# Optimization experiments

Measured on AMD Instinct MI355X. Metric: run time of the kernel, lower is better.

Reference implementation:

```python
import jax, jax.numpy as jnp
import numpy as np

HEAD_SIZE = 64


def setup_inputs() -> dict:
    key = jax.random.key(0)
    ks = jax.random.split(key, 4)
    B, S, H, D = 8, 4096, 768, HEAD_SIZE
    scale = 1.0 / np.sqrt(H)
    return {
        "x": jax.random.normal(ks[0], (B, S, H), dtype=jnp.float32),
        "Wq": jax.random.normal(ks[1], (H, D), dtype=jnp.float32) * scale,
        "bq": jnp.zeros((D,), dtype=jnp.float32),
        "Wk": jax.random.normal(ks[2], (H, D), dtype=jnp.float32) * scale,
        "bk": jnp.zeros((D,), dtype=jnp.float32),
        "Wv": jax.random.normal(ks[3], (H, D), dtype=jnp.float32) * scale,
        "bv": jnp.zeros((D,), dtype=jnp.float32),
    }


def reference(x, Wq, bq, Wk, bk, Wv, bv):
    # x: [B, S, H]
    B, S, H = x.shape
    D = Wq.shape[1]
    q = x @ Wq + bq  # [B, S, D]
    k = x @ Wk + bk
    v = x @ Wv + bv
    # naive full score matrix [B, S, S]
    scores = jnp.einsum("bsd,btd->bst", q, k)
    causal = jnp.tril(jnp.ones((S, S), dtype=bool))  # lower-triangular mask
    scores = jnp.where(causal[None, :, :], scores, -jnp.inf)
    attn = jax.nn.softmax(scores / jnp.sqrt(jnp.float32(D)), axis=-1)
    # dropout is identity in eval/deterministic reference
    out = jnp.einsum("bst,btd->bsd", attn, v)  # [B, S, D]
    return out
```

## Files before the change

kernel.cpp:

```cpp
#include <hip/hip_runtime.h>

typedef unsigned short u16;
typedef __bf16 bf16_t;
typedef bf16_t bf16x8 __attribute__((ext_vector_type(8)));
typedef float f32x4 __attribute__((ext_vector_type(4)));
typedef u16 u16x8 __attribute__((ext_vector_type(8)));
typedef u16 u16x4 __attribute__((ext_vector_type(4)));
typedef unsigned u32x4 __attribute__((ext_vector_type(4)));

#define B_ 8
#define S_ 4096
#define H_ 768
#define M_ (B_ * S_)

__device__ __forceinline__ u16 f2b(float f) {
  unsigned u = __float_as_uint(f);
  u += 0x7fffu + ((u >> 16) & 1u);
  return (u16)(u >> 16);
}

__device__ __forceinline__ void gl_lds16(const void* g, void* l) {
  __builtin_amdgcn_global_load_lds(
      (const __attribute__((address_space(1))) void*)g,
      (__attribute__((address_space(3))) void*)l, 16, 0, 0);
}

__global__ __launch_bounds__(256) void wconv_k(const float* __restrict__ Wq,
                                               const float* __restrict__ Wk,
                                               const float* __restrict__ Wv,
                                               u16* __restrict__ WbT) {
  __shared__ float wt[64 * 68];
  const int tid = threadIdx.x;
  int mat = blockIdx.x / 12;
  int k0 = (blockIdx.x % 12) * 64;
  const float* W = (mat == 0) ? Wq : ((mat == 1) ? Wk : Wv);
  int r = tid >> 2, c0 = (tid & 3) * 16;
  const float* src = W + (size_t)(k0 + r) * 64 + c0;
#pragma unroll
  for (int j = 0; j < 16; j += 4)
    *(float4*)&wt[r * 68 + c0 + j] = *(const float4*)(src + j);
  __syncthreads();
  int d = tid >> 2;
  u16* dst = WbT + (size_t)(mat * 64 + d) * 768 + k0 + c0;
  u16x8 o0, o1;
#pragma unroll
  for (int j = 0; j < 8; ++j) o0[j] = f2b(wt[(c0 + j) * 68 + d]);
#pragma unroll
  for (int j = 0; j < 8; ++j) o1[j] = f2b(wt[(c0 + 8 + j) * 68 + d]);
  *(u16x8*)dst = o0;
  *(u16x8*)(dst + 8) = o1;
}

__global__ __launch_bounds__(512) void qkv_k(const float* __restrict__ x,
                                             const u16* __restrict__ WbT,
                                             const float* __restrict__ bq,
                                             const float* __restrict__ bk,
                                             const float* __restrict__ bv,
                                             u16* __restrict__ qb,
                                             u16* __restrict__ kb,
                                             u16* __restrict__ vbT) {
  __shared__ __align__(16) u16 smem[2 * 5120 + 2 * 7680];
  const int tid = threadIdx.x;
  const int w = tid >> 6, ln = tid & 15, qd = (tid >> 4) & 3;
  const int rh = w >> 2;
  const int wc = w & 3;
  const int row0 = blockIdx.x * 128;

  const f32x4 z4 = {0.f, 0.f, 0.f, 0.f};
  f32x4 acc[4][3];
#pragma unroll
  for (int rt = 0; rt < 4; ++rt)
#pragma unroll
    for (int ct = 0; ct < 3; ++ct) acc[rt][ct] = z4;

  const int xr = tid >> 2, xc = (tid & 3) * 8;
  float4 xf0, xf1;
  u16x8 wf0, wf1;

  auto load_t = [&](int kt) {
    const float* sx = x + (size_t)(row0 + xr) * 768 + kt * 32 + xc;
    xf0 = *(const float4*)sx;
    xf1 = *(const float4*)(sx + 4);
    {
      int r = tid >> 2, off = (tid & 3) * 8;
      wf0 = *(const u16x8*)(WbT + (size_t)r * 768 + kt * 32 + off);
    }
    if (tid < 256) {
      int c = 512 + tid;
      int r = c >> 2, off = (c & 3) * 8;
      wf1 = *(const u16x8*)(WbT + (size_t)r * 768 + kt * 32 + off);
    }
  };

  load_t(0);
  for (int kt = 0; kt < 24; ++kt) {
    u16* xs = smem + (kt & 1) * 5120;
    u16* wsb = smem + 10240 + (kt & 1) * 7680;
    {
      u16x8 v;
      v[0] = f2b(xf0.x); v[1] = f2b(xf0.y); v[2] = f2b(xf0.z); v[3] = f2b(xf0.w);
      v[4] = f2b(xf1.x); v[5] = f2b(xf1.y); v[6] = f2b(xf1.z); v[7] = f2b(xf1.w);
      *(u16x8*)&xs[xr * 40 + xc] = v;
      {
        int r = tid >> 2, off = (tid & 3) * 8;
        *(u16x8*)&wsb[r * 40 + off] = wf0;
      }
      if (tid < 256) {
        int c = 512 + tid;
        int r = c >> 2, off = (c & 3) * 8;
        *(u16x8*)&wsb[r * 40 + off] = wf1;
      }
    }
    if (kt < 23) load_t(kt + 1);
    __syncthreads();
    bf16x8 af[4], bfr[3];
#pragma unroll
    for (int rt = 0; rt < 4; ++rt)
      af[rt] = *(const bf16x8*)&xs[(rh * 64 + rt * 16 + ln) * 40 + qd * 8];
#pragma unroll
    for (int ct = 0; ct < 3; ++ct)
      bfr[ct] = *(const bf16x8*)&wsb[(wc * 48 + ct * 16 + ln) * 40 + qd * 8];
#pragma unroll
    for (int rt = 0; rt < 4; ++rt)
#pragma unroll
      for (int ct = 0; ct < 3; ++ct)
        acc[rt][ct] = __builtin_amdgcn_mfma_f32_16x16x32_bf16(
            af[rt], bfr[ct], acc[rt][ct], 0, 0, 0);
  }
  __syncthreads();

  u16* vt = smem;
#pragma unroll
  for (int ct = 0; ct < 3; ++ct) {
    int col = wc * 48 + ct * 16 + ln;
    int mat = col >> 6, d = col & 63;
    if (mat < 2) {
      const float* bp = (mat == 0) ? bq : bk;
      u16* op = (mat == 0) ? qb : kb;
      float bias = bp[d];
      float scale = (mat == 0) ? 0.18033688011112042f : 1.0f;
#pragma unroll
      for (int rt = 0; rt < 4; ++rt)
#pragma unroll
        for (int r = 0; r < 4; ++r)
          op[(size_t)(row0 + rh * 64 + rt * 16 + qd * 4 + r) * 64 + d] =
              f2b((acc[rt][ct][r] + bias) * scale);
    } else {
      float bias = bv[d];
#pragma unroll
      for (int rt = 0; rt < 4; ++rt)
#pragma unroll
        for (int r = 0; r < 4; ++r)
          vt[d * 136 + rh * 64 + rt * 16 + qd * 4 + r] =
              f2b(acc[rt][ct][r] + bias);
    }
  }
  __syncthreads();
  {
    int d = tid >> 3, so = (tid & 7) * 16;
    int b = row0 >> 12, s0 = row0 & 4095;
    u16* dst = vbT + ((size_t)b * 64 + d) * 4096 + s0;
#pragma unroll
    for (int g = 0; g < 4; ++g) {
      int ts = so + g * 4;
      int tn = (ts & 0x40) | (ts & 0x23) | ((ts & 4) << 2) | ((ts & 0x18) >> 1);
      *(u16x4*)(dst + ts) = *(const u16x4*)&vt[d * 136 + tn];
    }
  }
}

__global__ __launch_bounds__(256) void attn_k(const u16* __restrict__ qb,
                                              const u16* __restrict__ kb,
                                              const u16* __restrict__ vbT,
                                              float* __restrict__ po,
                                              float* __restrict__ pl) {
  __shared__ __align__(16) u16 ks[2][4096];
  __shared__ __align__(16) u16 vs[2][4096];
  const int tid = threadIdx.x;
  const int wv = tid >> 6, ln = tid & 15, qd = (tid >> 4) & 3;
  const int id = blockIdx.x;
  const int b = id & 7;
  const int j = id >> 3;
  int qi = 31, acc = 0;
  for (;;) {
    int ncq = (2 * qi + 9) >> 3;
    if (acc + ncq <= j) { acc += ncq; --qi; } else break;
  }
  const int c = j - acc;
  const int ntiles = 2 * qi + 2;
  const int nc = (2 * qi + 9) >> 3;
  const int bas = ntiles / nc, rem = ntiles % nc;
  const int tstart = c * bas + (c < rem ? c : rem);
  const int tcount = bas + (c < rem ? 1 : 0);
  const int q0 = qi * 128;
  const int q0w = q0 + wv * 32;
  const int base = b * S_;
  const u16* kg = kb + (size_t)base * 64;
  const u16* vg = vbT + (size_t)b * 64 * 4096;

  bf16x8 qf[2][2];
#pragma unroll
  for (int qt = 0; qt < 2; ++qt) {
    const u16* qrow = qb + (size_t)(base + q0w + qt * 16 + ln) * 64;
    qf[qt][0] = *(const bf16x8*)(qrow + qd * 8);
    qf[qt][1] = *(const bf16x8*)(qrow + 32 + qd * 8);
  }
  const f32x4 z4 = {0.f, 0.f, 0.f, 0.f};
  f32x4 o0[4] = {z4, z4, z4, z4};
  f32x4 o1[4] = {z4, z4, z4, z4};
  float lq0 = 0.f, lq1 = 0.f;
  const int lr = (tid & 63) >> 3, csl = tid & 7;

  auto prefetch = [&](int bufi, int tile) {
    const u16* kt_ = kg + (size_t)tile * 4096;
    const u16* vt_ = vg + tile * 64;
#pragma unroll
    for (int i = 0; i < 2; ++i) {
      int r0 = wv * 16 + i * 8;
      int r = r0 + lr;
      int cc = csl ^ (r & 7);
      gl_lds16(kt_ + r * 64 + cc * 8, &ks[bufi][r0 * 64]);
      gl_lds16(vt_ + (size_t)r * 4096 + cc * 8, &vs[bufi][r0 * 64]);
    }
  };

  prefetch(0, tstart);
  int cur = 0;
  for (int it = 0; it < tcount; ++it) {
    asm volatile("s_waitcnt vmcnt(0)" ::: "memory");
    __builtin_amdgcn_s_barrier();
    if (it + 1 < tcount) prefetch(cur ^ 1, tstart + it + 1);
    const int t0a = (tstart + it) * 64;

    if (t0a <= q0w + 31) {
      f32x4 s0[4] = {z4, z4, z4, z4};
      f32x4 s1[4] = {z4, z4, z4, z4};
      __builtin_amdgcn_s_setprio(1);
#pragma unroll
      for (int kc = 0; kc < 2; ++kc) {
        int cs = (kc * 4 + qd) ^ (ln & 7);
#pragma unroll
        for (int nt = 0; nt < 4; ++nt) {
          bf16x8 kf = *(const bf16x8*)&ks[cur][(nt * 16 + ln) * 64 + cs * 8];
          s0[nt] = __builtin_amdgcn_mfma_f32_16x16x32_bf16(kf, qf[0][kc], s0[nt], 0, 0, 0);
          s1[nt] = __builtin_amdgcn_mfma_f32_16x16x32_bf16(kf, qf[1][kc], s1[nt], 0, 0, 0);
        }
      }
      __builtin_amdgcn_s_setprio(0);
      if (t0a + 63 > q0w) {
#pragma unroll
        for (int nt = 0; nt < 4; ++nt) {
          int tg = t0a + nt * 16 + qd * 4;
#pragma unroll
          for (int r = 0; r < 4; ++r) {
            if (tg + r > q0w + ln) s0[nt][r] = -INFINITY;
            if (tg + r > q0w + 16 + ln) s1[nt][r] = -INFINITY;
          }
        }
      }
      float p0[4][4], p1[4][4];
#pragma unroll
      for (int nt = 0; nt < 4; ++nt)
#pragma unroll
        for (int r = 0; r < 4; ++r) {
          p0[nt][r] = __builtin_amdgcn_exp2f(s0[nt][r]);
          p1[nt][r] = __builtin_amdgcn_exp2f(s1[nt][r]);
          lq0 += p0[nt][r];
          lq1 += p1[nt][r];
        }
      unsigned pk0[8], pk1[8];
#pragma unroll
      for (int i = 0; i < 8; ++i) {
        int nt = i >> 1, rb = (i & 1) * 2;
        asm("v_cvt_pk_bf16_f32 %0, %1, %2"
            : "=v"(pk0[i]) : "v"(p0[nt][rb]), "v"(p0[nt][rb + 1]));
        asm("v_cvt_pk_bf16_f32 %0, %1, %2"
            : "=v"(pk1[i]) : "v"(p1[nt][rb]), "v"(p1[nt][rb + 1]));
      }
      __builtin_amdgcn_s_setprio(1);
#pragma unroll
      for (int kc = 0; kc < 2; ++kc) {
        u32x4 w0 = {pk0[4 * kc], pk0[4 * kc + 1], pk0[4 * kc + 2], pk0[4 * kc + 3]};
        u32x4 w1 = {pk1[4 * kc], pk1[4 * kc + 1], pk1[4 * kc + 2], pk1[4 * kc + 3]};
        bf16x8 a0 = __builtin_bit_cast(bf16x8, w0);
        bf16x8 a1 = __builtin_bit_cast(bf16x8, w1);
        int cs = (kc * 4 + qd) ^ (ln & 7);
#pragma unroll
        for (int nt = 0; nt < 4; ++nt) {
          bf16x8 vf = *(const bf16x8*)&vs[cur][(nt * 16 + ln) * 64 + cs * 8];
          o0[nt] = __builtin_amdgcn_mfma_f32_16x16x32_bf16(a0, vf, o0[nt], 0, 0, 0);
          o1[nt] = __builtin_amdgcn_mfma_f32_16x16x32_bf16(a1, vf, o1[nt], 0, 0, 0);
        }
      }
      __builtin_amdgcn_s_setprio(0);
    }
    cur ^= 1;
  }

  lq0 += __shfl_xor(lq0, 16);
  lq0 += __shfl_xor(lq0, 32);
  lq1 += __shfl_xor(lq1, 16);
  lq1 += __shfl_xor(lq1, 32);

  float* op = po + (size_t)c * 2097152;
  float* lpt = pl + (size_t)c * 32768;
#pragma unroll
  for (int r = 0; r < 4; ++r) {
    int row0 = base + q0w + qd * 4 + r;
    int row1 = row0 + 16;
#pragma unroll
    for (int nt = 0; nt < 4; ++nt) {
      op[(size_t)row0 * 64 + nt * 16 + ln] = o0[nt][r];
      op[(size_t)row1 * 64 + nt * 16 + ln] = o1[nt][r];
    }
  }
  if (qd == 0) {
    lpt[base + q0w + ln] = lq0;
    lpt[base + q0w + 16 + ln] = lq1;
  }
}

__global__ __launch_bounds__(256) void comb_k(const float* __restrict__ po,
                                              const float* __restrict__ pl,
                                              float* __restrict__ out) {
  int idx = blockIdx.x * 256 + threadIdx.x;
  int r = idx >> 4, d0 = (idx & 15) * 4;
  int qi = (r & 4095) >> 7;
  int nc = (2 * qi + 9) >> 3;
  const float* p = po + (size_t)r * 64 + d0;
  float4 a = *(const float4*)p;
  float l = pl[r];
  for (int cc = 1; cc < nc; ++cc) {
    float4 t = *(const float4*)(p + (size_t)cc * 2097152);
    a.x += t.x; a.y += t.y; a.z += t.z; a.w += t.w;
    l += pl[r + cc * 32768];
  }
  float inv = 1.0f / l;
  a.x *= inv; a.y *= inv; a.z *= inv; a.w *= inv;
  *(float4*)(out + (size_t)r * 64 + d0) = a;
}

extern "C" void kernel_launch(void* const* d_in, const int* in_sizes, int n_in,
                              void* d_out, int out_size, void* d_ws, size_t ws_size,
                              hipStream_t stream) {
  const float* x  = (const float*)d_in[0];
  const float* Wq = (const float*)d_in[1];
  const float* bq = (const float*)d_in[2];
  const float* Wk = (const float*)d_in[3];
  const float* bk = (const float*)d_in[4];
  const float* Wv = (const float*)d_in[5];
  const float* bv = (const float*)d_in[6];
  float* out = (float*)d_out;

  char* wsp = (char*)d_ws;
  u16* WbT = (u16*)wsp;
  u16* qb  = (u16*)(wsp + 294912);
  u16* kb  = (u16*)(wsp + 4489216);
  u16* vbT = (u16*)(wsp + 8683520);
  float* po = (float*)(wsp + 12877824);
  float* pl = (float*)(wsp + 79986688);

  hipLaunchKernelGGL(wconv_k, dim3(36), dim3(256), 0, stream, Wq, Wk, Wv, WbT);
  hipLaunchKernelGGL(qkv_k, dim3(256), dim3(512), 0, stream,
                     x, WbT, bq, bk, bv, qb, kb, vbT);
  hipLaunchKernelGGL(attn_k, dim3(1152), dim3(256), 0, stream,
                     qb, kb, vbT, po, pl);
  hipLaunchKernelGGL(comb_k, dim3(2048), dim3(256), 0, stream,
                     po, pl, out);
}
```

Before: 208.0 us.

## Write single-chunk attention rows directly to output and deepen QKV load pipeline

When a query block's key range is handled by a single chunk (nc==1), the attention kernel now normalizes by the row sum and writes the final output directly, and the combine kernel skips those rows. This removes the partial-output write and re-read for those rows. Separately, the QKV projection loop double-buffers register prefetches two tiles ahead with explicit A/B registers, which uses more registers in exchange for more latency hiding.

After: 212.6 us. 1.02x slower.

```diff
diff --git a/kernel.cpp b/kernel.cpp
--- a/kernel.cpp
+++ b/kernel.cpp
@@ -74,45 +74,38 @@
     for (int ct = 0; ct < 3; ++ct) acc[rt][ct] = z4;
 
   const int xr = tid >> 2, xc = (tid & 3) * 8;
-  float4 xf0, xf1;
-  u16x8 wf0, wf1;
-
-  auto load_t = [&](int kt) {
+  const int wr = tid >> 2, woff = (tid & 3) * 8;
+  const int c2 = 512 + tid, wr2 = c2 >> 2, woff2 = (c2 & 3) * 8;
+
+  float4 xa0, xa1, xb0, xb1;
+  u16x8 wa0, wa1, wb0, wb1;
+
+  auto loadA = [&](int kt) {
     const float* sx = x + (size_t)(row0 + xr) * 768 + kt * 32 + xc;
-    xf0 = *(const float4*)sx;
-    xf1 = *(const float4*)(sx + 4);
-    {
-      int r = tid >> 2, off = (tid & 3) * 8;
-      wf0 = *(const u16x8*)(WbT + (size_t)r * 768 + kt * 32 + off);
-    }
-    if (tid < 256) {
-      int c = 512 + tid;
-      int r = c >> 2, off = (c & 3) * 8;
-      wf1 = *(const u16x8*)(WbT + (size_t)r * 768 + kt * 32 + off);
-    }
-  };
-
-  load_t(0);
-  for (int kt = 0; kt < 24; ++kt) {
-    u16* xs = smem + (kt & 1) * 5120;
-    u16* wsb = smem + 10240 + (kt & 1) * 7680;
-    {
-      u16x8 v;
-      v[0] = f2b(xf0.x); v[1] = f2b(xf0.y); v[2] = f2b(xf0.z); v[3] = f2b(xf0.w);
-      v[4] = f2b(xf1.x); v[5] = f2b(xf1.y); v[6] = f2b(xf1.z); v[7] = f2b(xf1.w);
-      *(u16x8*)&xs[xr * 40 + xc] = v;
-      {
-        int r = tid >> 2, off = (tid & 3) * 8;
-        *(u16x8*)&wsb[r * 40 + off] = wf0;
-      }
-      if (tid < 256) {
-        int c = 512 + tid;
-        int r = c >> 2, off = (c & 3) * 8;
-        *(u16x8*)&wsb[r * 40 + off] = wf1;
-      }
-    }
-    if (kt < 23) load_t(kt + 1);
-    __syncthreads();
+    xa0 = *(const float4*)sx;
+    xa1 = *(const float4*)(sx + 4);
+    wa0 = *(const u16x8*)(WbT + (size_t)wr * 768 + kt * 32 + woff);
+    if (tid < 256)
+      wa1 = *(const u16x8*)(WbT + (size_t)wr2 * 768 + kt * 32 + woff2);
+  };
+  auto loadB = [&](int kt) {
+    const float* sx = x + (size_t)(row0 + xr) * 768 + kt * 32 + xc;
+    xb0 = *(const float4*)sx;
+    xb1 = *(const float4*)(sx + 4);
+    wb0 = *(const u16x8*)(WbT + (size_t)wr * 768 + kt * 32 + woff);
+    if (tid < 256)
+      wb1 = *(const u16x8*)(WbT + (size_t)wr2 * 768 + kt * 32 + woff2);
+  };
+  auto stage = [&](u16* xs, u16* wsb, const float4& f0, const float4& f1,
+                   const u16x8& w0, const u16x8& w1) {
+    u16x8 v;
+    v[0] = f2b(f0.x); v[1] = f2b(f0.y); v[2] = f2b(f0.z); v[3] = f2b(f0.w);
+    v[4] = f2b(f1.x); v[5] = f2b(f1.y); v[6] = f2b(f1.z); v[7] = f2b(f1.w);
+    *(u16x8*)&xs[xr * 40 + xc] = v;
+    *(u16x8*)&wsb[wr * 40 + woff] = w0;
+    if (tid < 256) *(u16x8*)&wsb[wr2 * 40 + woff2] = w1;
+  };
+  auto compute = [&](const u16* xs, const u16* wsb) {
     bf16x8 af[4], bfr[3];
 #pragma unroll
     for (int rt = 0; rt < 4; ++rt)
@@ -126,6 +119,19 @@
       for (int ct = 0; ct < 3; ++ct)
         acc[rt][ct] = __builtin_amdgcn_mfma_f32_16x16x32_bf16(
             af[rt], bfr[ct], acc[rt][ct], 0, 0, 0);
+  };
+
+  loadA(0);
+  loadB(1);
+  for (int kt = 0; kt < 24; kt += 2) {
+    stage(smem, smem + 10240, xa0, xa1, wa0, wa1);
+    if (kt + 2 < 24) loadA(kt + 2);
+    __syncthreads();
+    compute(smem, smem + 10240);
+    stage(smem + 5120, smem + 10240 + 7680, xb0, xb1, wb0, wb1);
+    if (kt + 3 < 24) loadB(kt + 3);
+    __syncthreads();
+    compute(smem + 5120, smem + 10240 + 7680);
   }
   __syncthreads();
 
@@ -173,7 +179,8 @@
                                               const u16* __restrict__ kb,
                                               const u16* __restrict__ vbT,
                                               float* __restrict__ po,
-                                              float* __restrict__ pl) {
+                                              float* __restrict__ pl,
+                                              float* __restrict__ out) {
   __shared__ __align__(16) u16 ks[2][4096];
   __shared__ __align__(16) u16 vs[2][4096];
   const int tid = threadIdx.x;
@@ -302,6 +309,27 @@
   lq1 += __shfl_xor(lq1, 16);
   lq1 += __shfl_xor(lq1, 32);
 
+  if (nc == 1) {
+    float li0[4], li1[4];
+#pragma unroll
+    for (int r = 0; r < 4; ++r) {
+      li0[r] = __shfl(lq0, qd * 4 + r);
+      li1[r] = __shfl(lq1, qd * 4 + r);
+    }
+#pragma unroll
+    for (int r = 0; r < 4; ++r) {
+      int row0 = base + q0w + qd * 4 + r;
+      int row1 = row0 + 16;
+      float i0 = 1.0f / li0[r], i1 = 1.0f / li1[r];
+#pragma unroll
+      for (int nt = 0; nt < 4; ++nt) {
+        out[(size_t)row0 * 64 + nt * 16 + ln] = o0[nt][r] * i0;
+        out[(size_t)row1 * 64 + nt * 16 + ln] = o1[nt][r] * i1;
+      }
+    }
+    return;
+  }
+
   float* op = po + (size_t)c * 2097152;
   float* lpt = pl + (size_t)c * 32768;
 #pragma unroll
@@ -327,6 +355,7 @@
   int r = idx >> 4, d0 = (idx & 15) * 4;
   int qi = (r & 4095) >> 7;
   int nc = (2 * qi + 9) >> 3;
+  if (nc == 1) return;
   const float* p = po + (size_t)r * 64 + d0;
   float4 a = *(const float4*)p;
   float l = pl[r];
@@ -364,7 +393,7 @@
   hipLaunchKernelGGL(qkv_k, dim3(256), dim3(512), 0, stream,
                      x, WbT, bq, bk, bv, qb, kb, vbT);
   hipLaunchKernelGGL(attn_k, dim3(1152), dim3(256), 0, stream,
-                     qb, kb, vbT, po, pl);
+                     qb, kb, vbT, po, pl, out);
   hipLaunchKernelGGL(comb_k, dim3(2048), dim3(256), 0, stream,
                      po, pl, out);
 }
```
